# Kernel tuning notes

Measured on AMD Instinct MI355X. Metric: run time of the kernel, lower is better.

## Reference

```python
import jax, jax.numpy as jnp
import numpy as np

B, S, E, H = 4, 2048, 1024, 16
DH = E // H
NEG = -1e11


def setup_inputs() -> dict:
    key = jax.random.key(0)
    ks = jax.random.split(key, 9)
    scale = 1.0 / np.sqrt(E)
    return {
        "x": jax.random.normal(ks[0], (B, S, E), jnp.float32),
        "Wq": jax.random.normal(ks[1], (E, E), jnp.float32) * scale,
        "bq": jnp.zeros((E,), jnp.float32),
        "Wk": jax.random.normal(ks[2], (E, E), jnp.float32) * scale,
        "bk": jnp.zeros((E,), jnp.float32),
        "Wv": jax.random.normal(ks[3], (E, E), jnp.float32) * scale,
        "bv": jnp.zeros((E,), jnp.float32),
        "Wo": jax.random.normal(ks[4], (E, E), jnp.float32) * scale,
        "bo": jnp.zeros((E,), jnp.float32),
    }


def reference(x, Wq, bq, Wk, bk, Wv, bv, Wo, bo):
    # Faithful to the TF code: split_heads uses a pure reshape (B,S,E)->(B,H,S,DH),
    # which interleaves positions/features rather than transposing heads.
    def split_heads(e):
        return jnp.reshape(e, (-1, H, S, DH))

    q = split_heads(x @ Wq + bq)
    k = split_heads(x @ Wk + bk)
    v = split_heads(x @ Wv + bv)
    # scores: [B, H, S, S]
    w = jnp.einsum("bhqd,bhkd->bhqk", q, k) / np.sqrt(DH)
    mask = jnp.triu(jnp.ones((1, 1, S, S), jnp.float32), 1) * NEG
    w = w + mask
    w = jax.nn.softmax(w, axis=-1)
    z = jnp.einsum("bhqk,bhkd->bhqd", w, v)
    z = jnp.reshape(z, (-1, S, E))
    return z @ Wo + bo
```

## Files before the change

kernel.cpp:

```cpp
#include <hip/hip_runtime.h>
#include <hip/hip_bf16.h>

typedef unsigned short u16;
typedef __attribute__((ext_vector_type(8))) short bf16x8;
typedef __attribute__((ext_vector_type(4))) float f32x4;
typedef __attribute__((ext_vector_type(8))) unsigned short u16x8;
typedef __attribute__((ext_vector_type(4))) unsigned int u32x4;

#define MFMA16(a, b, c) __builtin_amdgcn_mfma_f32_16x16x32_bf16((a), (b), (c), 0, 0, 0)

#define SWZB(row) ((((row) & 3) | ((((row) >> 3) & 1) << 2)) << 4)

__device__ __forceinline__ u16 f2b(float f) {
  union { float f; unsigned u; } c; c.f = f;
  unsigned u = c.u;
  u += 0x7FFFu + ((u >> 16) & 1u);
  return (u16)(u >> 16);
}

__device__ __forceinline__ unsigned cvt_pk_bf16(float a, float b) {
  unsigned r;
  asm("v_cvt_pk_bf16_f32 %0, %1, %2" : "=v"(r) : "v"(a), "v"(b));
  return r;
}

__device__ __forceinline__ void gload_lds16(const u16* g, u16* l) {
  __builtin_amdgcn_global_load_lds(
      (__attribute__((address_space(1))) void*)(g),
      (__attribute__((address_space(3))) void*)(l),
      16, 0, 0);
}

__global__ __launch_bounds__(256) void convert_f32_bf16(const float* __restrict__ in,
                                                        u16* __restrict__ out) {
  int i = (blockIdx.x * 256 + threadIdx.x) * 8;
  float4 a = *(const float4*)&in[i];
  float4 b = *(const float4*)&in[i + 4];
  u16x8 o;
  o[0] = f2b(a.x); o[1] = f2b(a.y); o[2] = f2b(a.z); o[3] = f2b(a.w);
  o[4] = f2b(b.x); o[5] = f2b(b.y); o[6] = f2b(b.z); o[7] = f2b(b.w);
  *(u16x8*)&out[i] = o;
}

__global__ __launch_bounds__(256) void transpose_convert_w(
    const float* __restrict__ W0, const float* __restrict__ W1,
    const float* __restrict__ W2, const float* __restrict__ W3,
    u16* __restrict__ Wts) {
  __shared__ float t[32][33];
  int z = blockIdx.z;
  const float* W = (z == 0) ? W0 : (z == 1) ? W1 : (z == 2) ? W2 : W3;
  u16* Wt = Wts + (size_t)z * 1048576;
  int n0 = blockIdx.x * 32, k0 = blockIdx.y * 32;
  int tx = threadIdx.x, ty = threadIdx.y;
#pragma unroll
  for (int i = 0; i < 32; i += 8)
    t[ty + i][tx] = W[(size_t)(k0 + ty + i) * 1024 + n0 + tx];
  __syncthreads();
#pragma unroll
  for (int i = 0; i < 32; i += 8)
    Wt[(size_t)(n0 + ty + i) * 1024 + k0 + tx] = f2b(t[tx][ty + i]);
}

__global__ __launch_bounds__(256) void transpose_v(const u16* __restrict__ V,
                                                   u16* __restrict__ Vt) {
  __shared__ u16 t[32][33];
  int bh = blockIdx.z;
  int s0 = blockIdx.x * 32, d0 = blockIdx.y * 32;
  const u16* Vb = V + (size_t)bh * 131072;
  u16* Vtb = Vt + (size_t)bh * 131072;
  int tx = threadIdx.x, ty = threadIdx.y;
#pragma unroll
  for (int i = 0; i < 32; i += 8)
    t[ty + i][tx] = Vb[(s0 + ty + i) * 64 + d0 + tx];
  __syncthreads();
#pragma unroll
  for (int i = 0; i < 32; i += 8)
    Vtb[(d0 + ty + i) * 2048 + s0 + tx] = t[tx][ty + i];
}

template <bool F32OUT>
__global__ __launch_bounds__(256) void gemm_kernel(
    const u16* __restrict__ A, const u16* __restrict__ Wt0,
    const float* __restrict__ bias0, const float* __restrict__ bias1,
    const float* __restrict__ bias2,
    u16* __restrict__ outB, float* __restrict__ outF) {
  int z = blockIdx.z;
  const u16* Wt = Wt0 + (size_t)z * 1048576;
  const float* bias = (z == 0) ? bias0 : (z == 1) ? bias1 : bias2;
  u16* outb = outB + (size_t)z * 8388608;
  float oscale = (!F32OUT && z == 0) ? 0.125f * 1.44269504088896f : 1.0f;

  __shared__ u16 Alds[128 * 32];
  __shared__ u16 Blds[128 * 32];
  int tid = threadIdx.x;
  int lane = tid & 63, w = tid >> 6;
  int brow = blockIdx.x * 128;
  int bcol = blockIdx.y * 128;
  int wr = (w >> 1) * 64, wc = (w & 1) * 64;
  int r = lane & 15, half = lane >> 4;

  f32x4 acc[4][4] = {};
  int f0 = (w * 2 + 0) * 512 + lane * 8;
  int f1 = (w * 2 + 1) * 512 + lane * 8;
  const u16* Abase = A + (size_t)brow * 1024;
  const u16* Bbase = Wt + (size_t)bcol * 1024;

  for (int k0 = 0; k0 < 1024; k0 += 32) {
    gload_lds16(Abase + (size_t)(f0 >> 5) * 1024 + k0 + (f0 & 31), &Alds[(w * 2 + 0) * 512]);
    gload_lds16(Abase + (size_t)(f1 >> 5) * 1024 + k0 + (f1 & 31), &Alds[(w * 2 + 1) * 512]);
    gload_lds16(Bbase + (size_t)(f0 >> 5) * 1024 + k0 + (f0 & 31), &Blds[(w * 2 + 0) * 512]);
    gload_lds16(Bbase + (size_t)(f1 >> 5) * 1024 + k0 + (f1 & 31), &Blds[(w * 2 + 1) * 512]);
    __syncthreads();
    bf16x8 af[4], bf[4];
#pragma unroll
    for (int m = 0; m < 4; ++m)
      af[m] = *(const bf16x8*)&Alds[(wr + m * 16 + r) * 32 + half * 8];
#pragma unroll
    for (int n = 0; n < 4; ++n)
      bf[n] = *(const bf16x8*)&Blds[(wc + n * 16 + r) * 32 + half * 8];
#pragma unroll
    for (int m = 0; m < 4; ++m)
#pragma unroll
      for (int n = 0; n < 4; ++n)
        acc[m][n] = MFMA16(af[m], bf[n], acc[m][n]);
    __syncthreads();
  }
#pragma unroll
  for (int m = 0; m < 4; ++m) {
    int rowb = brow + wr + m * 16 + half * 4;
#pragma unroll
    for (int n = 0; n < 4; ++n) {
      int col = bcol + wc + n * 16 + r;
      float bv = bias[col];
#pragma unroll
      for (int j = 0; j < 4; ++j) {
        float v = (acc[m][n][j] + bv) * oscale;
        size_t idx = (size_t)(rowb + j) * 1024 + col;
        if (F32OUT) outF[idx] = v;
        else        outb[idx] = f2b(v);
      }
    }
  }
}

__device__ __forceinline__ void attn_stage(
    const u16* __restrict__ Kb, const u16* __restrict__ Vtb,
    u16* Kl, u16* Vl, int kb, int tid) {
  const int row0 = tid >> 3;
  const int cb0 = (tid & 7) << 4;
  const int row1 = row0 + 32;
  gload_lds16(Kb + (size_t)(kb + row0) * 64 + ((cb0 ^ SWZB(row0)) >> 1), Kl + tid * 8);
  gload_lds16(Kb + (size_t)(kb + row1) * 64 + ((cb0 ^ SWZB(row1)) >> 1), Kl + 2048 + tid * 8);
  gload_lds16(Vtb + (size_t)row0 * 2048 + kb + ((cb0 ^ SWZB(row0)) >> 1), Vl + tid * 8);
  gload_lds16(Vtb + (size_t)row1 * 2048 + kb + ((cb0 ^ SWZB(row1)) >> 1), Vl + 2048 + tid * 8);
}

__device__ __forceinline__ void attn_strip(
    const u16* __restrict__ Qb, const u16* __restrict__ Kb,
    const u16* __restrict__ Vtb, u16* __restrict__ Zb,
    u16 (*Kl)[4096], u16 (*Vl)[4096], int qrow, int nt, int tid) {
  const int lane = tid & 63;
  const int r = lane & 15, half = lane >> 4;
  const bf16x8 qf0 = *(const bf16x8*)&Qb[(qrow + r) * 64 + half * 8];
  const bf16x8 qf1 = *(const bf16x8*)&Qb[(qrow + r) * 64 + 32 + half * 8];
  const int q = qrow + r;
  f32x4 om[4] = {};
  float m_run = -1e30f, l_run = 0.f;

  __syncthreads();
  attn_stage(Kb, Vtb, Kl[0], Vl[0], 0, tid);
  int cur = 0;

  for (int kt = 0; kt < nt; ++kt) {
    const int kb = kt * 64;
    __syncthreads();
    if (kt + 1 < nt) attn_stage(Kb, Vtb, Kl[cur ^ 1], Vl[cur ^ 1], kb + 64, tid);
    const char* Kc = (const char*)Kl[cur];
    const char* Vc = (const char*)Vl[cur];

    f32x4 sT[2][2];
#pragma unroll
    for (int c = 0; c < 2; ++c)
#pragma unroll
      for (int t = 0; t < 2; ++t) {
        const int krow = c * 32 + ((r >> 2) << 3) + t * 4 + (r & 3);
        const char* krp = Kc + krow * 128;
        const bf16x8 kf0 = *(const bf16x8*)(krp + ((half * 16) ^ SWZB(krow)));
        const bf16x8 kf1 = *(const bf16x8*)(krp + ((64 + half * 16) ^ SWZB(krow)));
        f32x4 zacc = {};
        zacc = MFMA16(kf0, qf0, zacc);
        zacc = MFMA16(kf1, qf1, zacc);
        sT[c][t] = zacc;
      }
    if (kt == nt - 1) {
#pragma unroll
      for (int c = 0; c < 2; ++c)
#pragma unroll
        for (int t = 0; t < 2; ++t)
#pragma unroll
          for (int j = 0; j < 4; ++j)
            if (kb + c * 32 + half * 8 + t * 4 + j > q) sT[c][t][j] = -1e30f;
    }
    float mloc;
    {
      float a0 = fmaxf(fmaxf(sT[0][0][0], sT[0][0][1]), fmaxf(sT[0][0][2], sT[0][0][3]));
      float a1 = fmaxf(fmaxf(sT[0][1][0], sT[0][1][1]), fmaxf(sT[0][1][2], sT[0][1][3]));
      float a2 = fmaxf(fmaxf(sT[1][0][0], sT[1][0][1]), fmaxf(sT[1][0][2], sT[1][0][3]));
      float a3 = fmaxf(fmaxf(sT[1][1][0], sT[1][1][1]), fmaxf(sT[1][1][2], sT[1][1][3]));
      mloc = fmaxf(fmaxf(a0, a1), fmaxf(a2, a3));
    }
    if (__any(mloc > m_run + 8.0f)) {
      float mrow = fmaxf(mloc, __shfl_xor(mloc, 16));
      mrow = fmaxf(mrow, __shfl_xor(mrow, 32));
      const float nm = fmaxf(m_run, mrow);
      const float corr = __builtin_exp2f(m_run - nm);
      m_run = nm;
      l_run *= corr;
#pragma unroll
      for (int f = 0; f < 4; ++f)
#pragma unroll
        for (int j = 0; j < 4; ++j) om[f][j] *= corr;
    }
    const float mb = m_run;
    float lloc = 0.f;
    u32x4 pw[2];
#pragma unroll
    for (int c = 0; c < 2; ++c)
#pragma unroll
      for (int t = 0; t < 2; ++t) {
        const float e0 = __builtin_exp2f(sT[c][t][0] - mb);
        const float e1 = __builtin_exp2f(sT[c][t][1] - mb);
        const float e2 = __builtin_exp2f(sT[c][t][2] - mb);
        const float e3 = __builtin_exp2f(sT[c][t][3] - mb);
        lloc += (e0 + e1) + (e2 + e3);
        pw[c][t * 2 + 0] = cvt_pk_bf16(e0, e1);
        pw[c][t * 2 + 1] = cvt_pk_bf16(e2, e3);
      }
    l_run += lloc;
#pragma unroll
    for (int c = 0; c < 2; ++c) {
      const bf16x8 pb = __builtin_bit_cast(bf16x8, pw[c]);
#pragma unroll
      for (int f = 0; f < 4; ++f) {
        const int vrow = f * 16 + r;
        const bf16x8 vf = *(const bf16x8*)(Vc + vrow * 128 + ((c * 64 + half * 16) ^ SWZB(vrow)));
        om[f] = MFMA16(vf, pb, om[f]);
      }
    }
    cur ^= 1;
  }
  float lt = l_run;
  lt += __shfl_xor(lt, 16);
  lt += __shfl_xor(lt, 32);
  const float inv = 1.0f / lt;
#pragma unroll
  for (int f = 0; f < 4; ++f) {
    ushort4 st;
    st.x = f2b(om[f][0] * inv);
    st.y = f2b(om[f][1] * inv);
    st.z = f2b(om[f][2] * inv);
    st.w = f2b(om[f][3] * inv);
    *(ushort4*)&Zb[(size_t)q * 64 + f * 16 + half * 4] = st;
  }
}

__global__ __launch_bounds__(256) void attn_kernel(
    const u16* __restrict__ Q, const u16* __restrict__ K,
    const u16* __restrict__ Vt, u16* __restrict__ Z) {
  __shared__ u16 Kl[2][4096];
  __shared__ u16 Vl[2][4096];
  const int L = blockIdx.x;
  const int xcd = L & 7;
  const int i = L >> 3;
  const int bh = ((i >> 4) << 3) + xcd;
  const int x = i & 15;
  const int tid = threadIdx.x;
  const int w = tid >> 6;
  const u16* Qb = Q + (size_t)bh * 131072;
  const u16* Kb = K + (size_t)bh * 131072;
  const u16* Vb = Vt + (size_t)bh * 131072;
  u16* Zb = Z + (size_t)bh * 131072;
  attn_strip(Qb, Kb, Vb, Zb, Kl, Vl, x * 64 + w * 16, x + 1, tid);
  attn_strip(Qb, Kb, Vb, Zb, Kl, Vl, (31 - x) * 64 + w * 16, 32 - x, tid);
}

extern "C" void kernel_launch(void* const* d_in, const int* in_sizes, int n_in,
                              void* d_out, int out_size, void* d_ws, size_t ws_size,
                              hipStream_t stream) {
  (void)in_sizes; (void)n_in; (void)out_size; (void)ws_size;
  const float* x  = (const float*)d_in[0];
  const float* Wq = (const float*)d_in[1];
  const float* bq = (const float*)d_in[2];
  const float* Wk = (const float*)d_in[3];
  const float* bk = (const float*)d_in[4];
  const float* Wv = (const float*)d_in[5];
  const float* bv = (const float*)d_in[6];
  const float* Wo = (const float*)d_in[7];
  const float* bo = (const float*)d_in[8];
  float* out = (float*)d_out;

  char* ws = (char*)d_ws;
  u16* xb  = (u16*)(ws);
  u16* Wts = (u16*)(ws + 16777216);
  u16* Qb  = (u16*)(ws + 25165824);
  u16* Kb  = (u16*)(ws + 41943040);
  u16* Vb  = (u16*)(ws + 58720256);
  u16* Vtb = (u16*)(ws + 75497472);

  convert_f32_bf16<<<4096, 256, 0, stream>>>(x, xb);
  {
    dim3 g(32, 32, 4), b(32, 8);
    transpose_convert_w<<<g, b, 0, stream>>>(Wq, Wk, Wv, Wo, Wts);
  }
  {
    dim3 g(64, 8, 3), b(256);
    gemm_kernel<false><<<g, b, 0, stream>>>(xb, Wts, bq, bk, bv, Qb, nullptr);
  }
  {
    dim3 g(64, 2, 64), b(32, 8);
    transpose_v<<<g, b, 0, stream>>>(Vb, Vtb);
  }
  {
    dim3 g(1024), b(256);
    attn_kernel<<<g, b, 0, stream>>>(Qb, Kb, Vtb, xb );
  }
  {
    dim3 g(64, 8, 1), b(256);
    gemm_kernel<true><<<g, b, 0, stream>>>(xb, Wts + 3 * 1048576, bo, bo, bo, Qb, out);
  }
}
```

Before: 188.9 us.

## Split paired causal attention strips into separate blocks with heavy-first ordering

Each attention block previously handled two complementary query strips (x and 31-x) so every block had equal causal work. Now each block handles one 64-row strip, which doubles the grid to 2048 blocks, and a block-index remap alternates descending and ascending strip order so long strips tend to be scheduled early. The intent is more parallelism and dynamic load balancing across CUs. The cost is extra prologue overhead per block and a less even amount of work per block.

New measurement: 201.7 us. +6.8%, slower.

```diff
diff --git a/kernel.cpp b/kernel.cpp
--- a/kernel.cpp
+++ b/kernel.cpp
@@ -155,19 +155,37 @@
   gload_lds16(Vtb + (size_t)row1 * 2048 + kb + ((cb0 ^ SWZB(row1)) >> 1), Vl + 2048 + tid * 8);
 }
 
-__device__ __forceinline__ void attn_strip(
-    const u16* __restrict__ Qb, const u16* __restrict__ Kb,
-    const u16* __restrict__ Vtb, u16* __restrict__ Zb,
-    u16 (*Kl)[4096], u16 (*Vl)[4096], int qrow, int nt, int tid) {
+__global__ __launch_bounds__(256) void attn_kernel(
+    const u16* __restrict__ Q, const u16* __restrict__ K,
+    const u16* __restrict__ Vt, u16* __restrict__ Z) {
+  __shared__ u16 Kl[2][4096];
+  __shared__ u16 Vl[2][4096];
+  const int L = blockIdx.x;
+  const int xcd = L & 7;
+  const int t = L >> 3;
+  const int r8 = t >> 5;
+  const int c32 = t & 31;
+  const int u = (c32 + (r8 >> 1) * 8) & 31;
+  const int x = (r8 & 1) ? u : 31 - u;
+  const int bh = r8 * 8 + xcd;
+  const int nt = x + 1;
+
+  const int tid = threadIdx.x;
   const int lane = tid & 63;
+  const int w = tid >> 6;
   const int r = lane & 15, half = lane >> 4;
+  const u16* Qb = Q + (size_t)bh * 131072;
+  const u16* Kb = K + (size_t)bh * 131072;
+  const u16* Vtb = Vt + (size_t)bh * 131072;
+  u16* Zb = Z + (size_t)bh * 131072;
+
+  const int qrow = x * 64 + w * 16;
   const bf16x8 qf0 = *(const bf16x8*)&Qb[(qrow + r) * 64 + half * 8];
   const bf16x8 qf1 = *(const bf16x8*)&Qb[(qrow + r) * 64 + 32 + half * 8];
   const int q = qrow + r;
   f32x4 om[4] = {};
   float m_run = -1e30f, l_run = 0.f;
 
-  __syncthreads();
   attn_stage(Kb, Vtb, Kl[0], Vl[0], 0, tid);
   int cur = 0;
 
@@ -182,24 +200,24 @@
 #pragma unroll
     for (int c = 0; c < 2; ++c)
 #pragma unroll
-      for (int t = 0; t < 2; ++t) {
-        const int krow = c * 32 + ((r >> 2) << 3) + t * 4 + (r & 3);
+      for (int tt = 0; tt < 2; ++tt) {
+        const int krow = c * 32 + ((r >> 2) << 3) + tt * 4 + (r & 3);
         const char* krp = Kc + krow * 128;
         const bf16x8 kf0 = *(const bf16x8*)(krp + ((half * 16) ^ SWZB(krow)));
         const bf16x8 kf1 = *(const bf16x8*)(krp + ((64 + half * 16) ^ SWZB(krow)));
-        f32x4 zacc = {};
-        zacc = MFMA16(kf0, qf0, zacc);
-        zacc = MFMA16(kf1, qf1, zacc);
-        sT[c][t] = zacc;
+        f32x4 z = {};
+        z = MFMA16(kf0, qf0, z);
+        z = MFMA16(kf1, qf1, z);
+        sT[c][tt] = z;
       }
     if (kt == nt - 1) {
 #pragma unroll
       for (int c = 0; c < 2; ++c)
 #pragma unroll
-        for (int t = 0; t < 2; ++t)
+        for (int tt = 0; tt < 2; ++tt)
 #pragma unroll
           for (int j = 0; j < 4; ++j)
-            if (kb + c * 32 + half * 8 + t * 4 + j > q) sT[c][t][j] = -1e30f;
+            if (kb + c * 32 + half * 8 + tt * 4 + j > q) sT[c][tt][j] = -1e30f;
     }
     float mloc;
     {
@@ -227,14 +245,14 @@
 #pragma unroll
     for (int c = 0; c < 2; ++c)
 #pragma unroll
-      for (int t = 0; t < 2; ++t) {
-        const float e0 = __builtin_exp2f(sT[c][t][0] - mb);
-        const float e1 = __builtin_exp2f(sT[c][t][1] - mb);
-        const float e2 = __builtin_exp2f(sT[c][t][2] - mb);
-        const float e3 = __builtin_exp2f(sT[c][t][3] - mb);
+      for (int tt = 0; tt < 2; ++tt) {
+        const float e0 = __builtin_exp2f(sT[c][tt][0] - mb);
+        const float e1 = __builtin_exp2f(sT[c][tt][1] - mb);
+        const float e2 = __builtin_exp2f(sT[c][tt][2] - mb);
+        const float e3 = __builtin_exp2f(sT[c][tt][3] - mb);
         lloc += (e0 + e1) + (e2 + e3);
-        pw[c][t * 2 + 0] = cvt_pk_bf16(e0, e1);
-        pw[c][t * 2 + 1] = cvt_pk_bf16(e2, e3);
+        pw[c][tt * 2 + 0] = cvt_pk_bf16(e0, e1);
+        pw[c][tt * 2 + 1] = cvt_pk_bf16(e2, e3);
       }
     l_run += lloc;
 #pragma unroll
@@ -262,26 +280,6 @@
     st.w = f2b(om[f][3] * inv);
     *(ushort4*)&Zb[(size_t)q * 64 + f * 16 + half * 4] = st;
   }
-}
-
-__global__ __launch_bounds__(256) void attn_kernel(
-    const u16* __restrict__ Q, const u16* __restrict__ K,
-    const u16* __restrict__ Vt, u16* __restrict__ Z) {
-  __shared__ u16 Kl[2][4096];
-  __shared__ u16 Vl[2][4096];
-  const int L = blockIdx.x;
-  const int xcd = L & 7;
-  const int i = L >> 3;
-  const int bh = ((i >> 4) << 3) + xcd;
-  const int x = i & 15;
-  const int tid = threadIdx.x;
-  const int w = tid >> 6;
-  const u16* Qb = Q + (size_t)bh * 131072;
-  const u16* Kb = K + (size_t)bh * 131072;
-  const u16* Vb = Vt + (size_t)bh * 131072;
-  u16* Zb = Z + (size_t)bh * 131072;
-  attn_strip(Qb, Kb, Vb, Zb, Kl, Vl, x * 64 + w * 16, x + 1, tid);
-  attn_strip(Qb, Kb, Vb, Zb, Kl, Vl, (31 - x) * 64 + w * 16, 32 - x, tid);
 }
 
 extern "C" void kernel_launch(void* const* d_in, const int* in_sizes, int n_in,
@@ -321,7 +319,7 @@
     transpose_v<<<g, b, 0, stream>>>(Vb, Vtb);
   }
   {
-    dim3 g(1024), b(256);
+    dim3 g(2048), b(256);
     attn_kernel<<<g, b, 0, stream>>>(Qb, Kb, Vtb, xb );
   }
   {
```

## Add 256x256-tile pipelined GEMM kernel for QKV projection

Applied to the files above, without the earlier changes.

Replaces the generic 128-tile GEMM for the Q/K/V projections with a dedicated 512-thread kernel that computes 256x256 output tiles. It uses a double-buffered LDS (128 KB) filled by direct global-to-LDS loads issued between MFMA phases, with explicit waitcnt/barrier scheduling and s_setprio around MFMA bursts. The larger tile raises data reuse per LDS load and overlaps loads with compute, at the cost of fewer workgroups (384) and heavy register/LDS use that may limit occupancy. Minor renames and an add-to-or change in attention are cosmetic.

Measured after the change: 199.4 us. 5.6% more time.

```diff
diff --git a/kernel.cpp b/kernel.cpp
--- a/kernel.cpp
+++ b/kernel.cpp
@@ -143,6 +143,113 @@
   }
 }
 
+#define SG_A(U, h) do { \
+    gload_lds16(pA + (size_t)((h) * 128) * 1024 + (U) * 64, \
+                &LDSu[(((U) & 1) << 14) + ((h) << 13) + w * 512]); \
+    gload_lds16(pA + (size_t)((h) * 128 + 64) * 1024 + (U) * 64, \
+                &LDSu[(((U) & 1) << 14) + ((h) << 13) + 4096 + w * 512]); \
+  } while (0)
+#define SG_B(U, h) do { \
+    gload_lds16(pB + (size_t)((h) * 128) * 1024 + (U) * 64, \
+                &LDSu[32768 + (((U) & 1) << 14) + ((h) << 13) + w * 512]); \
+    gload_lds16(pB + (size_t)((h) * 128 + 64) * 1024 + (U) * 64, \
+                &LDSu[32768 + (((U) & 1) << 14) + ((h) << 13) + 4096 + w * 512]); \
+  } while (0)
+#define WGFENCE() asm volatile("" ::: "memory")
+
+__global__ __launch_bounds__(512, 2) void gemm256_qkv(
+    const u16* __restrict__ A, const u16* __restrict__ Wt0,
+    const float* __restrict__ bias0, const float* __restrict__ bias1,
+    const float* __restrict__ bias2, u16* __restrict__ outB) {
+  __shared__ u16 LDSu[65536];
+  const int z = blockIdx.z;
+  const u16* Wt = Wt0 + (size_t)z * 1048576;
+  const float* bias = (z == 0) ? bias0 : (z == 1) ? bias1 : bias2;
+  u16* outb = outB + (size_t)z * 8388608;
+  const float oscale = (z == 0) ? 0.125f * 1.44269504088896f : 1.0f;
+
+  const int tid = threadIdx.x;
+  const int w = tid >> 6, lane = tid & 63;
+  const int wm = w >> 2, wn = w & 3;
+  const int r = lane & 15, hh = lane >> 4;
+  const int brow = blockIdx.x * 256, bcol = blockIdx.y * 256;
+
+  const int swz2 = ((r >> 2) & 1) << 1;
+  const int sA0 = (hh ^ swz2) * 8;
+  const int sA1 = ((4 + hh) ^ swz2) * 8;
+  const int aBase = wm * 8192 + r * 64;
+  const int bBase = 32768 + (wn >> 1) * 8192 + ((wn & 1) * 64 + r) * 64;
+
+  const int srow = w * 8 + (lane >> 3);
+  const int sslot = (lane & 7) ^ (((lane >> 5) & 1) << 1);
+  const u16* pA = A  + (size_t)(brow + srow) * 1024 + sslot * 8;
+  const u16* pB = Wt + (size_t)(bcol + srow) * 1024 + sslot * 8;
+
+  f32x4 acc[8][4] = {};
+
+  SG_A(0, 0); SG_A(0, 1); SG_B(0, 0); SG_B(0, 1);
+  SG_A(1, 0); SG_A(1, 1); SG_B(1, 0); SG_B(1, 1);
+  asm volatile("s_waitcnt vmcnt(8)" ::: "memory");
+  __builtin_amdgcn_s_barrier();
+  WGFENCE();
+
+  for (int T = 0; T < 16; ++T) {
+    const int pT = (T & 1) << 14;
+    bf16x8 bfr[4][2];
+#pragma unroll
+    for (int q = 0; q < 4; ++q) {
+      bf16x8 a[2][2];
+      a[0][0] = *(const bf16x8*)&LDSu[pT + aBase + (2 * q) * 1024 + sA0];
+      a[0][1] = *(const bf16x8*)&LDSu[pT + aBase + (2 * q) * 1024 + sA1];
+      a[1][0] = *(const bf16x8*)&LDSu[pT + aBase + (2 * q + 1) * 1024 + sA0];
+      a[1][1] = *(const bf16x8*)&LDSu[pT + aBase + (2 * q + 1) * 1024 + sA1];
+      if (q == 0) {
+#pragma unroll
+        for (int n = 0; n < 4; ++n) {
+          bfr[n][0] = *(const bf16x8*)&LDSu[pT + bBase + n * 1024 + sA0];
+          bfr[n][1] = *(const bf16x8*)&LDSu[pT + bBase + n * 1024 + sA1];
+        }
+      }
+      WGFENCE();
+      __builtin_amdgcn_s_barrier();
+      WGFENCE();
+      if (q == 0)      { if (T >= 1 && T < 15) SG_A(T + 1, 0); }
+      else if (q == 1) { if (T >= 1 && T < 15) SG_A(T + 1, 1); }
+      else if (q == 2) { if (T < 14) SG_B(T + 2, 0); }
+      else {
+        if (T < 14) { SG_B(T + 2, 1);
+                      asm volatile("s_waitcnt vmcnt(4)" ::: "memory"); }
+        else        { asm volatile("s_waitcnt vmcnt(0)" ::: "memory"); }
+      }
+      __builtin_amdgcn_s_setprio(1);
+#pragma unroll
+      for (int n = 0; n < 4; ++n) {
+        acc[2 * q][n]     = MFMA16(a[0][0], bfr[n][0], acc[2 * q][n]);
+        acc[2 * q][n]     = MFMA16(a[0][1], bfr[n][1], acc[2 * q][n]);
+        acc[2 * q + 1][n] = MFMA16(a[1][0], bfr[n][0], acc[2 * q + 1][n]);
+        acc[2 * q + 1][n] = MFMA16(a[1][1], bfr[n][1], acc[2 * q + 1][n]);
+      }
+      __builtin_amdgcn_s_setprio(0);
+      WGFENCE();
+      __builtin_amdgcn_s_barrier();
+      WGFENCE();
+    }
+  }
+
+#pragma unroll
+  for (int m = 0; m < 8; ++m) {
+    const int row = brow + wm * 128 + m * 16 + hh * 4;
+#pragma unroll
+    for (int n = 0; n < 4; ++n) {
+      const int col = bcol + wn * 64 + n * 16 + r;
+      const float bv = bias[col];
+#pragma unroll
+      for (int j = 0; j < 4; ++j)
+        outb[(size_t)(row + j) * 1024 + col] = f2b((acc[m][n][j] + bv) * oscale);
+    }
+  }
+}
+
 __device__ __forceinline__ void attn_stage(
     const u16* __restrict__ Kb, const u16* __restrict__ Vtb,
     u16* Kl, u16* Vl, int kb, int tid) {
@@ -187,10 +294,10 @@
         const char* krp = Kc + krow * 128;
         const bf16x8 kf0 = *(const bf16x8*)(krp + ((half * 16) ^ SWZB(krow)));
         const bf16x8 kf1 = *(const bf16x8*)(krp + ((64 + half * 16) ^ SWZB(krow)));
-        f32x4 zacc = {};
-        zacc = MFMA16(kf0, qf0, zacc);
-        zacc = MFMA16(kf1, qf1, zacc);
-        sT[c][t] = zacc;
+        f32x4 zc = {};
+        zc = MFMA16(kf0, qf0, zc);
+        zc = MFMA16(kf1, qf1, zc);
+        sT[c][t] = zc;
       }
     if (kt == nt - 1) {
 #pragma unroll
@@ -272,7 +379,7 @@
   const int L = blockIdx.x;
   const int xcd = L & 7;
   const int i = L >> 3;
-  const int bh = ((i >> 4) << 3) + xcd;
+  const int bh = ((i >> 4) << 3) | xcd;
   const int x = i & 15;
   const int tid = threadIdx.x;
   const int w = tid >> 6;
@@ -313,8 +420,8 @@
     transpose_convert_w<<<g, b, 0, stream>>>(Wq, Wk, Wv, Wo, Wts);
   }
   {
-    dim3 g(64, 8, 3), b(256);
-    gemm_kernel<false><<<g, b, 0, stream>>>(xb, Wts, bq, bk, bv, Qb, nullptr);
+    dim3 g(32, 4, 3), b(512);
+    gemm256_qkv<<<g, b, 0, stream>>>(xb, Wts, bq, bk, bv, Qb);
   }
   {
     dim3 g(64, 2, 64), b(32, 8);
```

## Fuse V transpose into QKV GEMM epilogue and relax attention pipeline barrier

Applied to the files above, without the earlier changes.

The QKV GEMM epilogue for the V projection now writes directly into the transposed per-head Vt layout, which removes the separate transpose_v kernel and its extra round trip through global memory. The attention loop swaps __syncthreads for explicit s_barrier plus s_waitcnt vmcnt(4), so the next tile's async loads stay in flight while the current tile is consumed. The V epilogue writes become strided scattered 2-byte stores, which may coalesce poorly. The hand-written waitcnt also depends on exactly four outstanding loads per stage.

Result: slower. 221.8 us (+17.5%).

```diff
diff --git a/kernel.cpp b/kernel.cpp
--- a/kernel.cpp
+++ b/kernel.cpp
@@ -61,29 +61,12 @@
     Wt[(size_t)(n0 + ty + i) * 1024 + k0 + tx] = f2b(t[tx][ty + i]);
 }
 
-__global__ __launch_bounds__(256) void transpose_v(const u16* __restrict__ V,
-                                                   u16* __restrict__ Vt) {
-  __shared__ u16 t[32][33];
-  int bh = blockIdx.z;
-  int s0 = blockIdx.x * 32, d0 = blockIdx.y * 32;
-  const u16* Vb = V + (size_t)bh * 131072;
-  u16* Vtb = Vt + (size_t)bh * 131072;
-  int tx = threadIdx.x, ty = threadIdx.y;
-#pragma unroll
-  for (int i = 0; i < 32; i += 8)
-    t[ty + i][tx] = Vb[(s0 + ty + i) * 64 + d0 + tx];
-  __syncthreads();
-#pragma unroll
-  for (int i = 0; i < 32; i += 8)
-    Vtb[(d0 + ty + i) * 2048 + s0 + tx] = t[tx][ty + i];
-}
-
 template <bool F32OUT>
 __global__ __launch_bounds__(256) void gemm_kernel(
     const u16* __restrict__ A, const u16* __restrict__ Wt0,
     const float* __restrict__ bias0, const float* __restrict__ bias1,
     const float* __restrict__ bias2,
-    u16* __restrict__ outB, float* __restrict__ outF) {
+    u16* __restrict__ outB, u16* __restrict__ Vt, float* __restrict__ outF) {
   int z = blockIdx.z;
   const u16* Wt = Wt0 + (size_t)z * 1048576;
   const float* bias = (z == 0) ? bias0 : (z == 1) ? bias1 : bias2;
@@ -132,12 +115,23 @@
     for (int n = 0; n < 4; ++n) {
       int col = bcol + wc + n * 16 + r;
       float bv = bias[col];
-#pragma unroll
-      for (int j = 0; j < 4; ++j) {
-        float v = (acc[m][n][j] + bv) * oscale;
-        size_t idx = (size_t)(rowb + j) * 1024 + col;
-        if (F32OUT) outF[idx] = v;
-        else        outb[idx] = f2b(v);
+      if (!F32OUT && z == 2) {
+        const int b = rowb >> 11;
+        const int h = (rowb >> 7) & 15;
+        const int d = col & 63;
+        const int sbase = ((rowb & 127) << 4) | (col >> 6);
+        u16* vp = Vt + (size_t)(b * 16 + h) * 131072 + (size_t)d * 2048 + sbase;
+#pragma unroll
+        for (int j = 0; j < 4; ++j)
+          vp[j << 4] = f2b(acc[m][n][j] + bv);
+      } else {
+#pragma unroll
+        for (int j = 0; j < 4; ++j) {
+          float v = (acc[m][n][j] + bv) * oscale;
+          size_t idx = (size_t)(rowb + j) * 1024 + col;
+          if (F32OUT) outF[idx] = v;
+          else        outb[idx] = f2b(v);
+        }
       }
     }
   }
@@ -173,8 +167,14 @@
 
   for (int kt = 0; kt < nt; ++kt) {
     const int kb = kt * 64;
-    __syncthreads();
-    if (kt + 1 < nt) attn_stage(Kb, Vtb, Kl[cur ^ 1], Vl[cur ^ 1], kb + 64, tid);
+    asm volatile("s_barrier" ::: "memory");
+    if (kt + 1 < nt) {
+      attn_stage(Kb, Vtb, Kl[cur ^ 1], Vl[cur ^ 1], kb + 64, tid);
+      asm volatile("s_waitcnt vmcnt(4)" ::: "memory");
+    } else {
+      asm volatile("s_waitcnt vmcnt(0)" ::: "memory");
+    }
+    asm volatile("s_barrier" ::: "memory");
     const char* Kc = (const char*)Kl[cur];
     const char* Vc = (const char*)Vl[cur];
 
@@ -187,10 +187,10 @@
         const char* krp = Kc + krow * 128;
         const bf16x8 kf0 = *(const bf16x8*)(krp + ((half * 16) ^ SWZB(krow)));
         const bf16x8 kf1 = *(const bf16x8*)(krp + ((64 + half * 16) ^ SWZB(krow)));
-        f32x4 zacc = {};
-        zacc = MFMA16(kf0, qf0, zacc);
-        zacc = MFMA16(kf1, qf1, zacc);
-        sT[c][t] = zacc;
+        f32x4 zc = {};
+        zc = MFMA16(kf0, qf0, zc);
+        zc = MFMA16(kf1, qf1, zc);
+        sT[c][t] = zc;
       }
     if (kt == nt - 1) {
 #pragma unroll
@@ -272,7 +272,7 @@
   const int L = blockIdx.x;
   const int xcd = L & 7;
   const int i = L >> 3;
-  const int bh = ((i >> 4) << 3) + xcd;
+  const int bh = ((i >> 4) << 3) | xcd;
   const int x = i & 15;
   const int tid = threadIdx.x;
   const int w = tid >> 6;
@@ -304,8 +304,7 @@
   u16* Wts = (u16*)(ws + 16777216);
   u16* Qb  = (u16*)(ws + 25165824);
   u16* Kb  = (u16*)(ws + 41943040);
-  u16* Vb  = (u16*)(ws + 58720256);
-  u16* Vtb = (u16*)(ws + 75497472);
+  u16* Vtb = (u16*)(ws + 58720256);
 
   convert_f32_bf16<<<4096, 256, 0, stream>>>(x, xb);
   {
@@ -314,11 +313,7 @@
   }
   {
     dim3 g(64, 8, 3), b(256);
-    gemm_kernel<false><<<g, b, 0, stream>>>(xb, Wts, bq, bk, bv, Qb, nullptr);
-  }
-  {
-    dim3 g(64, 2, 64), b(32, 8);
-    transpose_v<<<g, b, 0, stream>>>(Vb, Vtb);
+    gemm_kernel<false><<<g, b, 0, stream>>>(xb, Wts, bq, bk, bv, Qb, Vtb, nullptr);
   }
   {
     dim3 g(1024), b(256);
@@ -326,6 +321,6 @@
   }
   {
     dim3 g(64, 8, 1), b(256);
-    gemm_kernel<true><<<g, b, 0, stream>>>(xb, Wts + 3 * 1048576, bo, bo, bo, Qb, out);
-  }
-}
+    gemm_kernel<true><<<g, b, 0, stream>>>(xb, Wts + 3 * 1048576, bo, bo, bo, Qb, Vtb, out);
+  }
+}
```
